# Optimization experiments

Measured on AMD Instinct MI355X. Metric: run time of the kernel, lower is better.

The kernel has to match this reference:

```python
import jax, jax.numpy as jnp
import numpy as np

D_MODEL = 1024
NUM_HEADS = 16
D_K = D_MODEL // NUM_HEADS  # 64
THETA = 10000.0
MAX_SEQ_LEN = 2048


def _trunc_normal(key, shape, std):
    # approximate trunc_normal_(mean=0, std, a=-3*std, b=3*std)
    u = jax.random.truncated_normal(key, -3.0, 3.0, shape, dtype=jnp.float32)
    return u * std


def setup_inputs() -> dict:
    key = jax.random.key(0)
    ks = jax.random.split(key, 5)
    x = jax.random.normal(ks[0], (2, 2048, D_MODEL), dtype=jnp.float32)
    token_positions = jnp.arange(2048, dtype=jnp.int64 if jax.config.jax_enable_x64 else jnp.int32)
    sigma = 2.0 / (D_MODEL + D_MODEL)
    Wq = _trunc_normal(ks[1], (D_MODEL, D_MODEL), sigma)
    Wk = _trunc_normal(ks[2], (D_MODEL, D_MODEL), sigma)
    Wv = _trunc_normal(ks[3], (D_MODEL, D_MODEL), sigma)
    Wo = _trunc_normal(ks[4], (D_MODEL, D_MODEL), sigma)
    return {"in_features": x, "Wq": Wq, "Wk": Wk, "Wv": Wv, "Wo": Wo,
            "token_positions": token_positions}


def _rope(x, cos_phi, sin_phi):
    # x: (..., seq, d_k); cos/sin: (seq, d_k//2)
    x_even = x[..., 0::2]
    x_odd = x[..., 1::2]
    y_even = x_even * cos_phi - x_odd * sin_phi
    y_odd = x_even * sin_phi + x_odd * cos_phi
    # interleave back
    y = jnp.stack([y_even, y_odd], axis=-1)
    return y.reshape(x.shape)


def reference(in_features, Wq, Wk, Wv, Wo, token_positions):
    b, s, d = in_features.shape
    h, dk = NUM_HEADS, D_K
    # projections: weight is (d_out, d_in)
    q = jnp.einsum('bsd,ed->bse', in_features, Wq)
    k = jnp.einsum('bsd,ed->bse', in_features, Wk)
    v = jnp.einsum('bsd,ed->bse', in_features, Wv)
    # split heads: (b, h, s, dk)
    q = q.reshape(b, s, h, dk).transpose(0, 2, 1, 3)
    k = k.reshape(b, s, h, dk).transpose(0, 2, 1, 3)
    v = v.reshape(b, s, h, dk).transpose(0, 2, 1, 3)
    # RoPE tables
    inv_freq = 1.0 / (THETA ** (jnp.arange(0, dk, 2, dtype=jnp.float32) / dk))
    phi = token_positions.astype(jnp.float32)[:, None] * inv_freq[None, :]  # (s, dk/2)
    cos_phi, sin_phi = jnp.cos(phi), jnp.sin(phi)
    q = _rope(q, cos_phi, sin_phi)
    k = _rope(k, cos_phi, sin_phi)
    # causal mask
    mask = jnp.tril(jnp.ones((s, s), dtype=bool))
    scores = jnp.einsum('bhqd,bhkd->bhqk', q, k) / jnp.sqrt(jnp.float32(dk))
    scores = jnp.where(mask, scores, -jnp.inf)
    attn = jax.nn.softmax(scores, axis=-1)
    out = jnp.einsum('bhqk,bhkd->bhqd', attn, v)
    out = out.transpose(0, 2, 1, 3).reshape(b, s, d)
    return jnp.einsum('bsd,ed->bse', out, Wo)
```

## Files before the change

kernel.cpp:

```cpp
#include <hip/hip_runtime.h>
#include <hip/hip_bf16.h>
#include <math.h>

#define S_  2048
#define DM_ 1024

typedef unsigned short u16;
typedef __attribute__((ext_vector_type(8))) short short8;
typedef __attribute__((ext_vector_type(4))) float f32x4;

__device__ __forceinline__ u16 f2bf(float f) {
  unsigned u = __float_as_uint(f);
  u += 0x7fffu + ((u >> 16) & 1u);
  return (u16)(u >> 16);
}
__device__ __forceinline__ float bf2f(u16 h) {
  return __uint_as_float((unsigned)h << 16);
}
__device__ __forceinline__ unsigned pack_bf2(float a, float b) {
  union { __hip_bfloat162 h2; unsigned u; } cv;
  cv.h2 = __float22bfloat162_rn(float2{a, b});
  return cv.u;
}
__device__ __forceinline__ void cp16(const void* g, void* l) {
  __builtin_amdgcn_global_load_lds(
      (const __attribute__((address_space(1))) unsigned*)(uintptr_t)g,
      (__attribute__((address_space(3))) unsigned*)(unsigned)(uintptr_t)l, 16, 0, 0);
}

struct CastArgs { const float* src[5]; u16* dst[5]; int n[5]; };

__global__ __launch_bounds__(256) void cast_kernel(CastArgs a) {
  const int z = blockIdx.y;
  const int i = (blockIdx.x * 256 + threadIdx.x) * 8;
  if (i >= a.n[z]) return;
  const float4* s = (const float4*)(a.src[z] + i);
  float4 v0 = s[0], v1 = s[1];
  short8 r;
  r[0] = (short)f2bf(v0.x); r[1] = (short)f2bf(v0.y);
  r[2] = (short)f2bf(v0.z); r[3] = (short)f2bf(v0.w);
  r[4] = (short)f2bf(v1.x); r[5] = (short)f2bf(v1.y);
  r[6] = (short)f2bf(v1.z); r[7] = (short)f2bf(v1.w);
  *(short8*)(a.dst[z] + i) = r;
}

struct GemmArgs { const u16* A; const u16* W[3]; void* out[3]; int modes; };

__global__ __launch_bounds__(256) void gemm_mfma(GemmArgs g) {
  __shared__ __align__(16) u16 As[2][4096];
  __shared__ __align__(16) u16 Bs[2][4096];
  const int tid = threadIdx.x, lane = tid & 63, w = tid >> 6;
  const int wr = w >> 1, wc = w & 1;
  const int z = blockIdx.z;
  const u16* __restrict__ A = g.A;
  const u16* __restrict__ W = g.W[z];
  const int m0 = blockIdx.y * 128, n0 = blockIdx.x * 128;

  const f32x4 fzero = {0.f, 0.f, 0.f, 0.f};
  f32x4 acc[4][4];
  #pragma unroll
  for (int i = 0; i < 4; i++)
    #pragma unroll
    for (int j = 0; j < 4; j++) acc[i][j] = fzero;

  const int c0 = tid >> 7;
  const int rs = tid & 127;
  const int fq = (lane >> 4) * 2048;
  const int fr = (lane & 15) * 16;

  const u16* Arow = A + (size_t)(m0 + rs) * 1024;
  const u16* Wrow = W + (size_t)(n0 + rs) * 1024;

  cp16(Arow + c0 * 8,       (char*)As[0] + w * 1024);
  cp16(Arow + (c0 + 2) * 8, (char*)As[0] + 4096 + w * 1024);
  cp16(Wrow + c0 * 8,       (char*)Bs[0] + w * 1024);
  cp16(Wrow + (c0 + 2) * 8, (char*)Bs[0] + 4096 + w * 1024);
  __syncthreads();

  for (int kt = 0; kt < 32; kt++) {
    const int cur = kt & 1, nxt = cur ^ 1;
    if (kt < 31) {
      const int k1 = (kt + 1) * 32;
      cp16(Arow + k1 + c0 * 8,       (char*)As[nxt] + w * 1024);
      cp16(Arow + k1 + (c0 + 2) * 8, (char*)As[nxt] + 4096 + w * 1024);
      cp16(Wrow + k1 + c0 * 8,       (char*)Bs[nxt] + w * 1024);
      cp16(Wrow + k1 + (c0 + 2) * 8, (char*)Bs[nxt] + 4096 + w * 1024);
    }

    short8 af[4], bf_[4];
    #pragma unroll
    for (int mt = 0; mt < 4; mt++)
      af[mt] = *(const short8*)((const char*)As[cur] + fq + (wr * 64 + mt * 16) * 16 + fr);
    #pragma unroll
    for (int nt = 0; nt < 4; nt++)
      bf_[nt] = *(const short8*)((const char*)Bs[cur] + fq + (wc * 64 + nt * 16) * 16 + fr);
    #pragma unroll
    for (int mt = 0; mt < 4; mt++)
      #pragma unroll
      for (int nt = 0; nt < 4; nt++)
        acc[mt][nt] = __builtin_amdgcn_mfma_f32_16x16x32_bf16(af[mt], bf_[nt], acc[mt][nt], 0, 0, 0);
    __syncthreads();
  }

  const int mode = (g.modes >> (2 * z)) & 3;
  const int rbase = m0 + wr * 64 + (lane >> 4) * 4;
  const int cbase = n0 + wc * 64 + (lane & 15);
  if (mode == 0) {
    u16* O = (u16*)g.out[z];
    #pragma unroll
    for (int mt = 0; mt < 4; mt++)
      #pragma unroll
      for (int nt = 0; nt < 4; nt++)
        #pragma unroll
        for (int r = 0; r < 4; r++)
          O[(size_t)(rbase + mt * 16 + r) * 1024 + cbase + nt * 16] = f2bf(acc[mt][nt][r]);
  } else if (mode == 1) {
    u16* O = (u16*)g.out[z];
    #pragma unroll
    for (int mt = 0; mt < 4; mt++)
      #pragma unroll
      for (int nt = 0; nt < 4; nt++) {
        int gr = rbase + mt * 16;
        int b = gr >> 11, s0 = gr & (S_ - 1);
        int gc = cbase + nt * 16;
        int h = gc >> 6, d = gc & 63;
        ushort4 v;
        v.x = f2bf(acc[mt][nt][0]); v.y = f2bf(acc[mt][nt][1]);
        v.z = f2bf(acc[mt][nt][2]); v.w = f2bf(acc[mt][nt][3]);
        *(ushort4*)&O[(size_t)((b * 16 + h) * 64 + d) * 2048 + s0] = v;
      }
  } else {
    float* O = (float*)g.out[z];
    #pragma unroll
    for (int mt = 0; mt < 4; mt++)
      #pragma unroll
      for (int nt = 0; nt < 4; nt++)
        #pragma unroll
        for (int r = 0; r < 4; r++)
          O[(size_t)(rbase + mt * 16 + r) * 1024 + cbase + nt * 16] = acc[mt][nt][r];
  }
}

__global__ __launch_bounds__(256) void rope_kernel(u16* qb, u16* kb, const int* __restrict__ tp) {
  const int isq = (blockIdx.y == 0);
  u16* p = isq ? qb : kb;
  const float outscale = isq ? 0.18033688011112042f : 1.0f;
  const int i = (blockIdx.x * 256 + threadIdx.x) * 8;
  const int s = (i >> 10) & (S_ - 1);
  const int d = i & 63;
  const float pos = (float)tp[s];
  short8 v = *(short8*)(p + i);
  #pragma unroll
  for (int j = 0; j < 4; j++) {
    float inv = exp2f(-(float)(d + 2 * j) * 0.20762050593046439f);
    float phi = pos * inv;
    float sn, cs;
    sincosf(phi, &sn, &cs);
    float xe = bf2f((u16)v[2 * j]), xo = bf2f((u16)v[2 * j + 1]);
    v[2 * j]     = (short)f2bf((xe * cs - xo * sn) * outscale);
    v[2 * j + 1] = (short)f2bf((xe * sn + xo * cs) * outscale);
  }
  *(short8*)(p + i) = v;
}

__global__ __launch_bounds__(512, 4) void attn_mfma(const u16* __restrict__ qb, const u16* __restrict__ kb,
                                                    const u16* __restrict__ vt, u16* __restrict__ ab) {
  __shared__ __align__(16) u16 Qs[2][4096];
  __shared__ __align__(16) u16 Ks[2][4096];
  __shared__ __align__(16) u16 Vs[2][4096];

  const int tid = threadIdx.x, lane = tid & 63, w = tid >> 6;
  const int v = w & 3, g = w >> 2;
  const int t = lane & 15, u = lane >> 4;
  const int bh = blockIdx.y, b = bh >> 4, h = bh & 15;
  const int i = blockIdx.x;
  const int qa = 31 - i;
  const int qbt = i;
  const int nk = 32 - i;
  const size_t qkb = (size_t)b * S_ * 1024 + h * 64;
  const size_t vtb = (size_t)bh * 64 * 2048;

  {
    const int qtile = g ? qbt : qa;
    cp16(qb + qkb + (size_t)(qtile * 64 + lane) * 1024 + v * 8,       (char*)Qs[g] + v * 1024);
    cp16(qb + qkb + (size_t)(qtile * 64 + lane) * 1024 + (v + 4) * 8, (char*)Qs[g] + 4096 + v * 1024);
  }
  cp16(kb + qkb + (size_t)lane * 1024 + w * 8, (char*)Ks[0] + w * 1024);
  cp16(vt + vtb + (size_t)lane * 2048 + w * 8, (char*)Vs[0] + w * 1024);
  __syncthreads();

  short8 aqA[2], aqP[2];
  #pragma unroll
  for (int ks = 0; ks < 2; ks++) {
    aqA[ks] = *(const short8*)((const char*)Qs[0] + (ks * 4 + u) * 1024 + (v * 16 + t) * 16);
    short8 bq = *(const short8*)((const char*)Qs[1] + (ks * 4 + u) * 1024 + (v * 16 + t) * 16);
    aqP[ks] = g ? bq : aqA[ks];
  }

  const f32x4 fzero = {0.f, 0.f, 0.f, 0.f};
  f32x4 oPrim[4], oSec[4];
  #pragma unroll
  for (int ct = 0; ct < 4; ct++) { oPrim[ct] = fzero; oSec[ct] = fzero; }
  float rsumP = 0.f, rsumS = 0.f;

  const int qprim = g ? qbt : qa;
  const int qrowP = qprim * 64 + v * 16 + t;
  const int qrowA = qa * 64 + v * 16 + t;

  for (int kt = 0; kt < nk; kt++) {
    const int cur = kt & 1, nxt = cur ^ 1;
    if (kt + 1 < nk) {
      cp16(kb + qkb + (size_t)((kt + 1) * 64 + lane) * 1024 + w * 8, (char*)Ks[nxt] + w * 1024);
      cp16(vt + vtb + (size_t)lane * 2048 + (kt + 1) * 64 + w * 8,   (char*)Vs[nxt] + w * 1024);
    }

    if (kt <= qbt) {
      f32x4 st[4] = {fzero, fzero, fzero, fzero};
      #pragma unroll
      for (int ks = 0; ks < 2; ks++)
        #pragma unroll
        for (int ct = 0; ct < 4; ct++) {
          short8 kf = *(const short8*)((const char*)Ks[cur] + (ks * 4 + u) * 1024 + (ct * 16 + t) * 16);
          st[ct] = __builtin_amdgcn_mfma_f32_16x16x32_bf16(kf, aqP[ks], st[ct], 0, 0, 0);
        }

      unsigned pb2[4][2];
      const bool diag = (kt == qprim);
      #pragma unroll
      for (int ct = 0; ct < 4; ct++) {
        float p[4];
        #pragma unroll
        for (int r = 0; r < 4; r++) {
          int key = kt * 64 + ct * 16 + 4 * u + r;
          float pv = exp2f(st[ct][r]);
          p[r] = (diag && key > qrowP) ? 0.f : pv;
          rsumP += p[r];
        }
        pb2[ct][0] = pack_bf2(p[0], p[1]);
        pb2[ct][1] = pack_bf2(p[2], p[3]);
      }

      #pragma unroll
      for (int ks = 0; ks < 2; ks++) {
        union { short8 s8; int i4[4]; } pf;
        #pragma unroll
        for (int jj = 0; jj < 4; jj++) {
          int src = 32 * (u & 1) + 16 * (jj >> 1) + t;
          int v0 = __shfl((int)pb2[ks * 2][jj & 1], src, 64);
          int v1 = __shfl((int)pb2[ks * 2 + 1][jj & 1], src, 64);
          pf.i4[jj] = (u >> 1) ? v1 : v0;
        }
        #pragma unroll
        for (int ct = 0; ct < 4; ct++) {
          short8 vf = *(const short8*)((const char*)Vs[cur] + (ks * 4 + u) * 1024 + (ct * 16 + t) * 16);
          oPrim[ct] = __builtin_amdgcn_mfma_f32_16x16x32_bf16(vf, pf.s8, oPrim[ct], 0, 0, 0);
        }
      }
    } else {
      f32x4 st2[2] = {fzero, fzero};
      #pragma unroll
      for (int ks = 0; ks < 2; ks++)
        #pragma unroll
        for (int c = 0; c < 2; c++) {
          short8 kf = *(const short8*)((const char*)Ks[cur] + (ks * 4 + u) * 1024 + ((2 * g + c) * 16 + t) * 16);
          st2[c] = __builtin_amdgcn_mfma_f32_16x16x32_bf16(kf, aqA[ks], st2[c], 0, 0, 0);
        }

      unsigned ph[2][2];
      float rs = 0.f;
      const bool diag = (kt == qa);
      #pragma unroll
      for (int c = 0; c < 2; c++) {
        float p[4];
        #pragma unroll
        for (int r = 0; r < 4; r++) {
          int key = kt * 64 + (2 * g + c) * 16 + 4 * u + r;
          float pv = exp2f(st2[c][r]);
          p[r] = (diag && key > qrowA) ? 0.f : pv;
          rs += p[r];
        }
        ph[c][0] = pack_bf2(p[0], p[1]);
        ph[c][1] = pack_bf2(p[2], p[3]);
      }

      union { short8 s8; int i4[4]; } pf;
      #pragma unroll
      for (int jj = 0; jj < 4; jj++) {
        int src = 32 * (u & 1) + 16 * (jj >> 1) + t;
        int v0 = __shfl((int)ph[0][jj & 1], src, 64);
        int v1 = __shfl((int)ph[1][jj & 1], src, 64);
        pf.i4[jj] = (u >> 1) ? v1 : v0;
      }
      if (g) {
        rsumS += rs;
        #pragma unroll
        for (int ct = 0; ct < 4; ct++) {
          short8 vf = *(const short8*)((const char*)Vs[cur] + (4 + u) * 1024 + (ct * 16 + t) * 16);
          oSec[ct] = __builtin_amdgcn_mfma_f32_16x16x32_bf16(vf, pf.s8, oSec[ct], 0, 0, 0);
        }
      } else {
        rsumP += rs;
        #pragma unroll
        for (int ct = 0; ct < 4; ct++) {
          short8 vf = *(const short8*)((const char*)Vs[cur] + u * 1024 + (ct * 16 + t) * 16);
          oPrim[ct] = __builtin_amdgcn_mfma_f32_16x16x32_bf16(vf, pf.s8, oPrim[ct], 0, 0, 0);
        }
      }
    }
    __syncthreads();
  }

  float* dmpO = (float*)Ks;
  float* dmpR = (float*)Vs;
  if (g) {
    #pragma unroll
    for (int ct = 0; ct < 4; ct++)
      *(f32x4*)&dmpO[(size_t)(v * 64 + lane) * 16 + ct * 4] = oSec[ct];
    dmpR[v * 64 + lane] = rsumS;
    float rs = rsumP;
    rs += __shfl_xor(rs, 16, 64);
    rs += __shfl_xor(rs, 32, 64);
    const float inv = 1.0f / rs;
    #pragma unroll
    for (int ct = 0; ct < 4; ct++) {
      ushort4 vv;
      vv.x = f2bf(oPrim[ct][0] * inv); vv.y = f2bf(oPrim[ct][1] * inv);
      vv.z = f2bf(oPrim[ct][2] * inv); vv.w = f2bf(oPrim[ct][3] * inv);
      *(ushort4*)&ab[((size_t)b * S_ + qrowP) * 1024 + h * 64 + ct * 16 + 4 * u] = vv;
    }
  }
  __syncthreads();
  if (!g) {
    #pragma unroll
    for (int ct = 0; ct < 4; ct++) {
      f32x4 add = *(const f32x4*)&dmpO[(size_t)(v * 64 + lane) * 16 + ct * 4];
      oPrim[ct] += add;
    }
    float rs = rsumP + dmpR[v * 64 + lane];
    rs += __shfl_xor(rs, 16, 64);
    rs += __shfl_xor(rs, 32, 64);
    const float inv = 1.0f / rs;
    #pragma unroll
    for (int ct = 0; ct < 4; ct++) {
      ushort4 vv;
      vv.x = f2bf(oPrim[ct][0] * inv); vv.y = f2bf(oPrim[ct][1] * inv);
      vv.z = f2bf(oPrim[ct][2] * inv); vv.w = f2bf(oPrim[ct][3] * inv);
      *(ushort4*)&ab[((size_t)b * S_ + qrowA) * 1024 + h * 64 + ct * 16 + 4 * u] = vv;
    }
  }
}

extern "C" void kernel_launch(void* const* d_in, const int* in_sizes, int n_in,
                              void* d_out, int out_size, void* d_ws, size_t ws_size,
                              hipStream_t stream) {
  const float* x  = (const float*)d_in[0];
  const float* Wq = (const float*)d_in[1];
  const float* Wk = (const float*)d_in[2];
  const float* Wv = (const float*)d_in[3];
  const float* Wo = (const float*)d_in[4];
  const int*   tp = (const int*)d_in[5];
  float* out = (float*)d_out;

  char* ws = (char*)d_ws;
  u16* xb  = (u16*)(ws);
  u16* wqb = (u16*)(ws + (8 << 20));
  u16* wkb = (u16*)(ws + (10 << 20));
  u16* wvb = (u16*)(ws + (12 << 20));
  u16* wob = (u16*)(ws + (14 << 20));
  u16* qbuf = (u16*)(ws + (16 << 20));
  u16* kbuf = (u16*)(ws + (24 << 20));
  u16* vtb  = (u16*)(ws + (32 << 20));
  u16* abuf = (u16*)(ws + (40 << 20));

  CastArgs ca;
  ca.src[0] = x;  ca.dst[0] = xb;  ca.n[0] = 2 * S_ * DM_;
  ca.src[1] = Wq; ca.dst[1] = wqb; ca.n[1] = DM_ * DM_;
  ca.src[2] = Wk; ca.dst[2] = wkb; ca.n[2] = DM_ * DM_;
  ca.src[3] = Wv; ca.dst[3] = wvb; ca.n[3] = DM_ * DM_;
  ca.src[4] = Wo; ca.dst[4] = wob; ca.n[4] = DM_ * DM_;
  cast_kernel<<<dim3(2048, 5), 256, 0, stream>>>(ca);

  GemmArgs gq;
  gq.A = xb;
  gq.W[0] = wqb; gq.W[1] = wkb; gq.W[2] = wvb;
  gq.out[0] = qbuf; gq.out[1] = kbuf; gq.out[2] = vtb;
  gq.modes = (1 << 4);
  gemm_mfma<<<dim3(8, 32, 3), 256, 0, stream>>>(gq);

  rope_kernel<<<dim3(2048, 2), 256, 0, stream>>>(qbuf, kbuf, tp);

  attn_mfma<<<dim3(16, 32), 512, 0, stream>>>(qbuf, kbuf, vtb, abuf);

  GemmArgs go;
  go.A = abuf;
  go.W[0] = wob; go.W[1] = wob; go.W[2] = wob;
  go.out[0] = out; go.out[1] = out; go.out[2] = out;
  go.modes = 2;
  gemm_mfma<<<dim3(8, 32, 1), 256, 0, stream>>>(go);
}
```

Measured before the change: 227.4 us.

## Load GEMM MFMA fragments directly from global memory, dropping LDS staging

The projection GEMM no longer stages A and W tiles through double-buffered shared memory with barriers. Each wave now loads its own MFMA fragments straight from global memory into registers, with a two-deep register prefetch across k-steps. This removes LDS traffic and the per-iteration __syncthreads, but gives up operand sharing between waves, so each tile row is fetched from global/L2 twice and the loads are strided 16-byte accesses.

```diff
diff --git a/kernel.cpp b/kernel.cpp
--- a/kernel.cpp
+++ b/kernel.cpp
@@ -47,14 +47,14 @@
 struct GemmArgs { const u16* A; const u16* W[3]; void* out[3]; int modes; };
 
 __global__ __launch_bounds__(256) void gemm_mfma(GemmArgs g) {
-  __shared__ __align__(16) u16 As[2][4096];
-  __shared__ __align__(16) u16 Bs[2][4096];
   const int tid = threadIdx.x, lane = tid & 63, w = tid >> 6;
   const int wr = w >> 1, wc = w & 1;
+  const int t = lane & 15, u = lane >> 4;
   const int z = blockIdx.z;
-  const u16* __restrict__ A = g.A;
-  const u16* __restrict__ W = g.W[z];
   const int m0 = blockIdx.y * 128, n0 = blockIdx.x * 128;
+
+  const u16* __restrict__ Abase = g.A    + (size_t)(m0 + wr * 64 + t) * 1024 + u * 8;
+  const u16* __restrict__ Wbase = g.W[z] + (size_t)(n0 + wc * 64 + t) * 1024 + u * 8;
 
   const f32x4 fzero = {0.f, 0.f, 0.f, 0.f};
   f32x4 acc[4][4];
@@ -63,43 +63,38 @@
     #pragma unroll
     for (int j = 0; j < 4; j++) acc[i][j] = fzero;
 
-  const int c0 = tid >> 7;
-  const int rs = tid & 127;
-  const int fq = (lane >> 4) * 2048;
-  const int fr = (lane & 15) * 16;
-
-  const u16* Arow = A + (size_t)(m0 + rs) * 1024;
-  const u16* Wrow = W + (size_t)(n0 + rs) * 1024;
-
-  cp16(Arow + c0 * 8,       (char*)As[0] + w * 1024);
-  cp16(Arow + (c0 + 2) * 8, (char*)As[0] + 4096 + w * 1024);
-  cp16(Wrow + c0 * 8,       (char*)Bs[0] + w * 1024);
-  cp16(Wrow + (c0 + 2) * 8, (char*)Bs[0] + 4096 + w * 1024);
-  __syncthreads();
-
-  for (int kt = 0; kt < 32; kt++) {
-    const int cur = kt & 1, nxt = cur ^ 1;
-    if (kt < 31) {
-      const int k1 = (kt + 1) * 32;
-      cp16(Arow + k1 + c0 * 8,       (char*)As[nxt] + w * 1024);
-      cp16(Arow + k1 + (c0 + 2) * 8, (char*)As[nxt] + 4096 + w * 1024);
-      cp16(Wrow + k1 + c0 * 8,       (char*)Bs[nxt] + w * 1024);
-      cp16(Wrow + k1 + (c0 + 2) * 8, (char*)Bs[nxt] + 4096 + w * 1024);
-    }
-
-    short8 af[4], bf_[4];
-    #pragma unroll
-    for (int mt = 0; mt < 4; mt++)
-      af[mt] = *(const short8*)((const char*)As[cur] + fq + (wr * 64 + mt * 16) * 16 + fr);
-    #pragma unroll
-    for (int nt = 0; nt < 4; nt++)
-      bf_[nt] = *(const short8*)((const char*)Bs[cur] + fq + (wc * 64 + nt * 16) * 16 + fr);
+  short8 fa[2][4], fb[2][4];
+
+  #pragma unroll
+  for (int mt = 0; mt < 4; mt++) {
+    fa[0][mt] = *(const short8*)(Abase + mt * 16384);
+    fb[0][mt] = *(const short8*)(Wbase + mt * 16384);
+  }
+
+  #pragma unroll 1
+  for (int kt = 0; kt < 32; kt += 2) {
+    #pragma unroll
+    for (int mt = 0; mt < 4; mt++) {
+      fa[1][mt] = *(const short8*)(Abase + (kt + 1) * 32 + mt * 16384);
+      fb[1][mt] = *(const short8*)(Wbase + (kt + 1) * 32 + mt * 16384);
+    }
     #pragma unroll
     for (int mt = 0; mt < 4; mt++)
       #pragma unroll
       for (int nt = 0; nt < 4; nt++)
-        acc[mt][nt] = __builtin_amdgcn_mfma_f32_16x16x32_bf16(af[mt], bf_[nt], acc[mt][nt], 0, 0, 0);
-    __syncthreads();
+        acc[mt][nt] = __builtin_amdgcn_mfma_f32_16x16x32_bf16(fa[0][mt], fb[0][nt], acc[mt][nt], 0, 0, 0);
+    if (kt + 2 < 32) {
+      #pragma unroll
+      for (int mt = 0; mt < 4; mt++) {
+        fa[0][mt] = *(const short8*)(Abase + (kt + 2) * 32 + mt * 16384);
+        fb[0][mt] = *(const short8*)(Wbase + (kt + 2) * 32 + mt * 16384);
+      }
+    }
+    #pragma unroll
+    for (int mt = 0; mt < 4; mt++)
+      #pragma unroll
+      for (int nt = 0; nt < 4; nt++)
+        acc[mt][nt] = __builtin_amdgcn_mfma_f32_16x16x32_bf16(fa[1][mt], fb[1][nt], acc[mt][nt], 0, 0, 0);
   }
 
   const int mode = (g.modes >> (2 * z)) & 3;
```

After: 262.3 us. 15.3% more time.
